# Performance work log

Hardware: AMD Instinct MI355X
Metric: run time of the kernel (lower is better)

The kernel has to match this reference:

```python
import jax, jax.numpy as jnp
import numpy as np

N_NODES = 50000
N_EDGES = 800000
HIDDEN = 128
NUM_LAYERS = 3
NEG_SLOPE = 0.2  # PyG GATConv default leaky_relu slope


def setup_inputs() -> dict:
    key = jax.random.key(0)
    ks = jax.random.split(key, 10)
    d = HIDDEN
    glorot = 1.0 / np.sqrt(d)
    inp = {
        "x": jax.random.normal(ks[0], (N_NODES, d), dtype=jnp.float32),
        "edge_index": jax.random.randint(ks[1], (2, N_EDGES), 0, N_NODES, dtype=jnp.int32),
        "edge_mask": jax.random.uniform(ks[2], (N_EDGES,), dtype=jnp.float32),
        # GATConv params (heads=1)
        "W_gat": jax.random.normal(ks[3], (d, d), dtype=jnp.float32) * glorot,
        "a_src": jax.random.normal(ks[4], (d,), dtype=jnp.float32) * glorot,
        "a_dst": jax.random.normal(ks[5], (d,), dtype=jnp.float32) * glorot,
        "b_gat": jnp.zeros((d,), dtype=jnp.float32),
        # Stacked GCNConv params
        "W_gcn": jax.random.normal(ks[6], (NUM_LAYERS, d, d), dtype=jnp.float32) * glorot,
        "b_gcn": jnp.zeros((NUM_LAYERS, d), dtype=jnp.float32),
    }
    return inp


def _seg_softmax(e, seg, n):
    m = jax.ops.segment_max(e, seg, num_segments=n)
    p = jnp.exp(e - m[seg])
    s = jax.ops.segment_sum(p, seg, num_segments=n)
    return p / s[seg]


def reference(x, edge_index, edge_mask, W_gat, a_src, a_dst, b_gat, W_gcn, b_gcn):
    N = x.shape[0]
    loops = jnp.arange(N, dtype=edge_index.dtype)
    src = jnp.concatenate([edge_index[0], loops])  # [E+N] with self loops
    dst = jnp.concatenate([edge_index[1], loops])

    # --- GATConv (heads=1, add_self_loops=True); edge_attr ignored (edge_dim=None) ---
    xp = x @ W_gat                                      # [N, d]
    e = jax.nn.leaky_relu((xp @ a_src)[src] + (xp @ a_dst)[dst], NEG_SLOPE)
    alpha = _seg_softmax(e, dst, N)                     # segment softmax over incoming edges
    h = jax.ops.segment_sum(alpha[:, None] * xp[src], dst, num_segments=N) + b_gat

    # --- GCN normalization with edge_mask as edge_weight (self-loop weight = 1) ---
    w = jnp.concatenate([edge_mask, jnp.ones((N,), dtype=edge_mask.dtype)])
    deg = jax.ops.segment_sum(w, dst, num_segments=N)
    dinv = jnp.where(deg > 0, jax.lax.rsqrt(jnp.maximum(deg, 1e-12)), 0.0)
    norm = dinv[src] * w * dinv[dst]                    # [E+N]

    outs = [h]
    for l in range(NUM_LAYERS):
        z = outs[-1] @ W_gcn[l]                         # [N, d]
        z = jax.ops.segment_sum(norm[:, None] * z[src], dst, num_segments=N) + b_gcn[l]
        outs.append(jax.nn.relu(z))

    # JumpingKnowledge 'max': elementwise max over layer outputs
    return jnp.max(jnp.stack(outs, axis=0), axis=0)
```

## Files before the change

### kernel.cpp

```cpp
#include <hip/hip_runtime.h>

#define HIDDEN 128
#define NEG_SLOPE 0.2f
#define P_SORT 256

typedef unsigned short ushort_t;
typedef __attribute__((ext_vector_type(8))) short short8;
typedef __attribute__((ext_vector_type(4))) float floatx4;

static inline size_t align_up(size_t x, size_t a){ return (x + a - 1) & ~(a - 1); }

__device__ __forceinline__ ushort_t f2b(float f){
  unsigned u = __float_as_uint(f);
  unsigned r = (u + 0x7FFFu + ((u >> 16) & 1u)) >> 16;
  return (ushort_t)r;
}

__device__ __forceinline__ void fma8(float* acc, uint4 v, float a){
  acc[0] += a * __uint_as_float(v.x << 16);
  acc[1] += a * __uint_as_float(v.x & 0xFFFF0000u);
  acc[2] += a * __uint_as_float(v.y << 16);
  acc[3] += a * __uint_as_float(v.y & 0xFFFF0000u);
  acc[4] += a * __uint_as_float(v.z << 16);
  acc[5] += a * __uint_as_float(v.z & 0xFFFF0000u);
  acc[6] += a * __uint_as_float(v.w << 16);
  acc[7] += a * __uint_as_float(v.w & 0xFFFF0000u);
}

__device__ __forceinline__ uint4 pack8(const float* f){
  uint4 u;
  u.x = (unsigned)f2b(f[0]) | ((unsigned)f2b(f[1]) << 16);
  u.y = (unsigned)f2b(f[2]) | ((unsigned)f2b(f[3]) << 16);
  u.z = (unsigned)f2b(f[4]) | ((unsigned)f2b(f[5]) << 16);
  u.w = (unsigned)f2b(f[6]) | ((unsigned)f2b(f[7]) << 16);
  return u;
}


__global__ __launch_bounds__(256) void k_b1cnt(const int* __restrict__ dst,
                                               int* __restrict__ bcnt,
                                               int E, int epb, int nbkt){
  __shared__ unsigned c[256];
  int t = threadIdx.x;
  c[t] = 0;
  __syncthreads();
  int e0 = blockIdx.x * epb;
  int e1 = min(E, e0 + epb);
  for (int e = e0 + t; e < e1; e += 256) atomicAdd(&c[dst[e] >> 8], 1u);
  __syncthreads();
  if (t < nbkt) bcnt[t * P_SORT + blockIdx.x] = (int)c[t];
}

__global__ void k_scan1(const int* __restrict__ in, int* __restrict__ incl,
                        int* __restrict__ blockSums, int M){
  __shared__ int sd[256];
  int t = threadIdx.x;
  int i = blockIdx.x*256 + t;
  int v = (i < M) ? in[i] : 0;
  sd[t] = v; __syncthreads();
  for (int off = 1; off < 256; off <<= 1){
    int add = (t >= off) ? sd[t-off] : 0;
    __syncthreads();
    sd[t] += add;
    __syncthreads();
  }
  if (i < M) incl[i] = sd[t];
  if (t == 255) blockSums[blockIdx.x] = sd[255];
}

__global__ void k_scan2(const int* __restrict__ blockSums, int* __restrict__ blockOffs, int nb){
  __shared__ int sd[256];
  __shared__ int carry;
  int t = threadIdx.x;
  if (t == 0) carry = 0;
  __syncthreads();
  for (int base = 0; base < nb; base += 256){
    int i = base + t;
    int v = (i < nb) ? blockSums[i] : 0;
    sd[t] = v; __syncthreads();
    for (int off = 1; off < 256; off <<= 1){
      int add = (t >= off) ? sd[t-off] : 0;
      __syncthreads();
      sd[t] += add;
      __syncthreads();
    }
    if (i < nb) blockOffs[i] = carry + sd[t] - v;
    __syncthreads();
    if (t == 0) carry += sd[255];
    __syncthreads();
  }
}

__global__ void k_scanex(int* __restrict__ arr, const int* __restrict__ in,
                         const int* __restrict__ blockOffs, int M){
  int i = blockIdx.x*256 + threadIdx.x;
  if (i < M) arr[i] = arr[i] - in[i] + blockOffs[blockIdx.x];
}

__global__ __launch_bounds__(256) void k_b1place(const int* __restrict__ src,
                                                 const int* __restrict__ dst,
                                                 const float* __restrict__ w,
                                                 const int* __restrict__ ebase,
                                                 unsigned* __restrict__ tpk,
                                                 float* __restrict__ tw,
                                                 int E, int epb){
  __shared__ unsigned c[256];
  int t = threadIdx.x;
  c[t] = 0;
  __syncthreads();
  int e0 = blockIdx.x * epb;
  int e1 = min(E, e0 + epb);
  for (int e = e0 + t; e < e1; e += 256){
    int d = dst[e];
    int b = d >> 8;
    unsigned r = atomicAdd(&c[b], 1u);
    int pos = ebase[b * P_SORT + blockIdx.x] + (int)r;
    tpk[pos] = (unsigned)src[e] | ((unsigned)(d & 255) << 16);
    tw[pos]  = w[e];
  }
}

__global__ __launch_bounds__(256) void k_b2(const unsigned* __restrict__ tpk,
                                            const float* __restrict__ tw,
                                            const int* __restrict__ ebase,
                                            int* __restrict__ col_src,
                                            float* __restrict__ col_w,
                                            int* __restrict__ rowp,
                                            float* __restrict__ dinv,
                                            int N, int E, int nbkt){
  __shared__ unsigned hcnt[256];
  __shared__ int sd[256];
  __shared__ int lofs[256];
  __shared__ unsigned rcnt[256];
  __shared__ float wsum[256];
  int b = blockIdx.x, t = threadIdx.x;
  int e0 = ebase[b * P_SORT];
  int e1 = (b + 1 < nbkt) ? ebase[(b + 1) * P_SORT] : E;
  hcnt[t] = 0; rcnt[t] = 0; wsum[t] = 0.f;
  __syncthreads();
  for (int e = e0 + t; e < e1; e += 256) atomicAdd(&hcnt[(tpk[e] >> 16) & 255u], 1u);
  __syncthreads();
  int v = (int)hcnt[t];
  sd[t] = v; __syncthreads();
  for (int off = 1; off < 256; off <<= 1){
    int add = (t >= off) ? sd[t-off] : 0;
    __syncthreads();
    sd[t] += add;
    __syncthreads();
  }
  lofs[t] = sd[t] - v;
  int node = b*256 + t;
  if (node < N) rowp[node] = e0 + sd[t] - v;
  if (b == 0 && t == 0) rowp[N] = E;
  __syncthreads();
  for (int e = e0 + t; e < e1; e += 256){
    unsigned pk = tpk[e];
    float wv = tw[e];
    unsigned dl = (pk >> 16) & 255u;
    unsigned r = atomicAdd(&rcnt[dl], 1u);
    int pos = e0 + lofs[dl] + (int)r;
    col_src[pos] = (int)(pk & 0xFFFFu);
    col_w[pos]   = wv;
    atomicAdd(&wsum[dl], wv);
  }
  __syncthreads();
  if (node < N) dinv[node] = rsqrtf(wsum[t] + 1.0f);
}


__global__ void k_cast_x(const float* __restrict__ x, unsigned* __restrict__ xb, long n2){
  long i = (long)blockIdx.x*256 + threadIdx.x;
  if (i >= n2) return;
  float2 v = ((const float2*)x)[i];
  xb[i] = (unsigned)f2b(v.x) | ((unsigned)f2b(v.y) << 16);
}

__global__ void k_cast_w(const float* __restrict__ Wg, const float* __restrict__ Wc,
                         ushort_t* __restrict__ Wt){
  int i = blockIdx.x*256 + threadIdx.x;
  int mat = i >> 14, idx = i & 16383;
  int k = idx >> 7, n = idx & 127;
  float v = (mat == 0) ? Wg[idx] : Wc[(mat-1)*16384 + idx];
  Wt[mat*16384 + n*128 + k] = f2b(v);
}

__global__ __launch_bounds__(256) void k_gemm(const ushort_t* __restrict__ A,
                                              const ushort_t* __restrict__ Wt,
                                              ushort_t* __restrict__ C, int M){
  int wave = threadIdx.x >> 6, l = threadIdx.x & 63;
  int q = l >> 4, lm = l & 15;
  int rowBase = blockIdx.x*128 + wave*32;
  floatx4 acc[2][8];
  #pragma unroll
  for (int mt = 0; mt < 2; mt++)
    #pragma unroll
    for (int nt = 0; nt < 8; nt++) acc[mt][nt] = (floatx4){0.f,0.f,0.f,0.f};

  #pragma unroll
  for (int kc = 0; kc < 4; kc++){
    int k0 = kc*32 + q*8;
    short8 a[2];
    #pragma unroll
    for (int mt = 0; mt < 2; mt++){
      long r = rowBase + mt*16 + lm;
      if (r < M) a[mt] = *(const short8*)(A + r*128 + k0);
      else       a[mt] = (short8){0,0,0,0,0,0,0,0};
    }
    #pragma unroll
    for (int nt = 0; nt < 8; nt++){
      short8 b = *(const short8*)(Wt + (nt*16 + lm)*128 + k0);
      acc[0][nt] = __builtin_amdgcn_mfma_f32_16x16x32_bf16(a[0], b, acc[0][nt], 0, 0, 0);
      acc[1][nt] = __builtin_amdgcn_mfma_f32_16x16x32_bf16(a[1], b, acc[1][nt], 0, 0, 0);
    }
  }
  #pragma unroll
  for (int mt = 0; mt < 2; mt++){
    #pragma unroll
    for (int r = 0; r < 4; r++){
      long row = rowBase + mt*16 + q*4 + r;
      if (row < M){
        #pragma unroll
        for (int nt = 0; nt < 8; nt++)
          C[row*128 + nt*16 + lm] = f2b(acc[mt][nt][r]);
      }
    }
  }
}

__global__ void k_sdots(const unsigned* __restrict__ xb, const float* __restrict__ a_src,
                        const float* __restrict__ a_dst, const float* __restrict__ dinv,
                        float2* __restrict__ attr, float* __restrict__ sdst, int N){
  int n = blockIdx.x*4 + (threadIdx.x >> 6);
  int lane = threadIdx.x & 63;
  if (n >= N) return;
  unsigned w = xb[(size_t)n*64 + lane];
  float v0 = __uint_as_float(w << 16);
  float v1 = __uint_as_float(w & 0xFFFF0000u);
  float2 as = ((const float2*)a_src)[lane];
  float2 ad = ((const float2*)a_dst)[lane];
  float ps = v0*as.x + v1*as.y;
  float pd = v0*ad.x + v1*ad.y;
  #pragma unroll
  for (int off = 32; off >= 1; off >>= 1){
    ps += __shfl_xor(ps, off, 64);
    pd += __shfl_xor(pd, off, 64);
  }
  if (lane == 0){
    attr[n] = make_float2(ps, dinv[n]);
    sdst[n] = pd;
  }
}

__global__ void k_post(const int* __restrict__ rowp, const int* __restrict__ col_src,
                       const float* __restrict__ col_w, const float2* __restrict__ attr,
                       const float* __restrict__ sdst, const float* __restrict__ dinv,
                       int2* __restrict__ col_en, int2* __restrict__ col_ea,
                       float* __restrict__ selfa, int N){
  int n = blockIdx.x*4 + (threadIdx.x >> 6);
  int l = threadIdx.x & 63;
  if (n >= N) return;
  int rs = rowp[n], re = rowp[n+1];
  float dn = dinv[n], sdd = sdst[n];
  float es = attr[n].x + sdd;
  es = (es >= 0.f) ? es : NEG_SLOPE*es;
  float m = es;
  float lg[3];
  int r = 0;
  for (int j = rs + l; j < re; j += 64, r++){
    int s = col_src[j];
    float w = col_w[j];
    float2 a = attr[s];
    col_en[j] = make_int2(s, __float_as_int(a.y * w * dn));
    float ee = a.x + sdd;
    ee = (ee >= 0.f) ? ee : NEG_SLOPE*ee;
    if (r < 3) lg[r] = ee;
    m = fmaxf(m, ee);
  }
  #pragma unroll
  for (int off = 32; off >= 1; off >>= 1) m = fmaxf(m, __shfl_xor(m, off, 64));
  float ps = 0.f;
  r = 0;
  for (int j = rs + l; j < re; j += 64, r++){
    float ee;
    if (r < 3) ee = lg[r];
    else {
      float2 a = attr[col_en[j].x];
      ee = a.x + sdd;
      ee = (ee >= 0.f) ? ee : NEG_SLOPE*ee;
    }
    ps += __expf(ee - m);
  }
  #pragma unroll
  for (int off = 32; off >= 1; off >>= 1) ps += __shfl_xor(ps, off, 64);
  ps += __expf(es - m);
  float inv = 1.f / ps;
  r = 0;
  for (int j = rs + l; j < re; j += 64, r++){
    float ee;
    if (r < 3) ee = lg[r];
    else {
      float2 a = attr[col_en[j].x];
      ee = a.x + sdd;
      ee = (ee >= 0.f) ? ee : NEG_SLOPE*ee;
    }
    col_ea[j] = make_int2(col_en[j].x, __float_as_int(__expf(ee - m) * inv));
  }
  if (l == 0) selfa[n] = __expf(es - m) * inv;
}

template<int MODE>
__global__ __launch_bounds__(256) void k_agg(const ushort_t* __restrict__ feat,
                                             const int* __restrict__ rowp,
                                             const int2* __restrict__ col,
                                             const float* __restrict__ selfc,
                                             const float* __restrict__ bias,
                                             ushort_t* __restrict__ out,
                                             float* __restrict__ y, int N){
  int n = blockIdx.x*4 + (threadIdx.x >> 6);
  if (n >= N) return;
  int l = threadIdx.x & 63;
  int sub = l >> 4, q = l & 15;
  int rs = rowp[n], re = rowp[n+1];
  const uint4* f16 = (const uint4*)feat;
  float acc[8] = {0.f,0.f,0.f,0.f,0.f,0.f,0.f,0.f};
  for (int base = rs; base < re; base += 8){
    int ea = base + sub;
    int eb = ea + 4;
    int ca = min(ea, re-1), cb = min(eb, re-1);
    int2 pa = col[ca];
    int2 pb = col[cb];
    float aa = (ea < re) ? __int_as_float(pa.y) : 0.f;
    float ab = (eb < re) ? __int_as_float(pb.y) : 0.f;
    uint4 va = f16[(size_t)pa.x*16 + q];
    uint4 vb = f16[(size_t)pb.x*16 + q];
    fma8(acc, va, aa);
    fma8(acc, vb, ab);
  }
  #pragma unroll
  for (int j = 0; j < 8; j++){
    acc[j] += __shfl_xor(acc[j], 16, 64);
    acc[j] += __shfl_xor(acc[j], 32, 64);
  }
  if (sub == 0){
    float sc = selfc[n];
    if (MODE == 1) sc = sc * sc;
    uint4 v = f16[(size_t)n*16 + q];
    fma8(acc, v, sc);
    float4 b0 = ((const float4*)bias)[q*2];
    float4 b1 = ((const float4*)bias)[q*2 + 1];
    acc[0]+=b0.x; acc[1]+=b0.y; acc[2]+=b0.z; acc[3]+=b0.w;
    acc[4]+=b1.x; acc[5]+=b1.y; acc[6]+=b1.z; acc[7]+=b1.w;
    if (MODE == 1){
      #pragma unroll
      for (int j = 0; j < 8; j++) acc[j] = fmaxf(acc[j], 0.f);
    }
    ((uint4*)out)[(size_t)n*16 + q] = pack8(acc);
    float4* y4 = (float4*)y;
    size_t yi = (size_t)n*32 + q*2;
    float4 n0 = make_float4(acc[0], acc[1], acc[2], acc[3]);
    float4 n1 = make_float4(acc[4], acc[5], acc[6], acc[7]);
    if (MODE == 0){
      y4[yi] = n0; y4[yi+1] = n1;
    } else {
      float4 y0 = y4[yi], y1 = y4[yi+1];
      y0.x=fmaxf(y0.x,n0.x); y0.y=fmaxf(y0.y,n0.y); y0.z=fmaxf(y0.z,n0.z); y0.w=fmaxf(y0.w,n0.w);
      y1.x=fmaxf(y1.x,n1.x); y1.y=fmaxf(y1.y,n1.y); y1.z=fmaxf(y1.z,n1.z); y1.w=fmaxf(y1.w,n1.w);
      y4[yi] = y0; y4[yi+1] = y1;
    }
  }
}

extern "C" void kernel_launch(void* const* d_in, const int* in_sizes, int n_in,
                              void* d_out, int out_size, void* d_ws, size_t ws_size,
                              hipStream_t stream){
  const float* x      = (const float*)d_in[0];
  const int*   eidx   = (const int*)d_in[1];
  const float* emask  = (const float*)d_in[2];
  const float* W_gat  = (const float*)d_in[3];
  const float* a_src  = (const float*)d_in[4];
  const float* a_dst  = (const float*)d_in[5];
  const float* b_gat  = (const float*)d_in[6];
  const float* W_gcn  = (const float*)d_in[7];
  const float* b_gcn  = (const float*)d_in[8];
  int N = in_sizes[0] / HIDDEN;
  int E = in_sizes[1] / 2;
  const int* src = eidx;
  const int* dst = eidx + E;

  char* p = (char*)d_ws;
  auto carve = [&](size_t bytes)->char*{ char* q = p; p += align_up(bytes, 512); return q; };
  ushort_t* xb   = (ushort_t*)carve((size_t)N*HIDDEN*2);
  ushort_t* zb   = (ushort_t*)carve((size_t)N*HIDDEN*2);
  ushort_t* hb   = (ushort_t*)carve((size_t)N*HIDDEN*2);
  ushort_t* Wt   = (ushort_t*)carve((size_t)4*HIDDEN*HIDDEN*2);
  float2* attr   = (float2*)carve((size_t)N*8);
  float* sdst    = (float*)carve((size_t)N*4);
  float* dinv    = (float*)carve((size_t)N*4);
  float* selfa   = (float*)carve((size_t)N*4);
  int*   rowp    = (int*)  carve((size_t)(N+1)*4);
  int*   col_src = (int*)  carve((size_t)E*4);
  float* col_w   = (float*)carve((size_t)E*4);
  int2*  col_en  = (int2*) carve((size_t)E*8);
  int2*  col_ea  = (int2*) carve((size_t)E*8);
  unsigned* tpk  = (unsigned*)carve((size_t)E*4);
  float* tw      = (float*)carve((size_t)E*4);
  int nbkt = (N + 255) >> 8;
  int M    = nbkt * P_SORT;
  int*   bcnt  = (int*)carve((size_t)M*4);
  int*   ebase = (int*)carve((size_t)M*4);
  int nbs = (M + 255) / 256;
  int*   blockSums = (int*)carve((size_t)nbs*4);
  int*   blockOffs = (int*)carve((size_t)nbs*4);
  (void)ws_size; (void)n_in; (void)out_size;

  int epb = (E + P_SORT - 1) / P_SORT;
  int gb  = (N + 127) / 128;
  int nwb = (N + 3) / 4;
  long n2 = (long)N*64;
  int cb  = (int)((n2 + 255) / 256);

  k_b1cnt  <<<P_SORT, 256, 0, stream>>>(dst, bcnt, E, epb, nbkt);
  k_scan1  <<<nbs, 256, 0, stream>>>(bcnt, ebase, blockSums, M);
  k_scan2  <<<1,   256, 0, stream>>>(blockSums, blockOffs, nbs);
  k_scanex <<<nbs, 256, 0, stream>>>(ebase, bcnt, blockOffs, M);
  k_b1place<<<P_SORT, 256, 0, stream>>>(src, dst, emask, ebase, tpk, tw, E, epb);
  k_b2     <<<nbkt, 256, 0, stream>>>(tpk, tw, ebase, col_src, col_w, rowp, dinv, N, E, nbkt);

  k_cast_x<<<cb, 256, 0, stream>>>(x, (unsigned*)xb, n2);
  k_cast_w<<<(4*HIDDEN*HIDDEN)/256, 256, 0, stream>>>(W_gat, W_gcn, Wt);

  k_gemm <<<gb, 256, 0, stream>>>(xb, Wt, zb, N);
  k_sdots<<<nwb,256, 0, stream>>>((const unsigned*)zb, a_src, a_dst, dinv, attr, sdst, N);
  k_post <<<nwb,256, 0, stream>>>(rowp, col_src, col_w, attr, sdst, dinv,
                                  col_en, col_ea, selfa, N);

  k_agg<0><<<nwb, 256, 0, stream>>>(zb, rowp, col_ea, selfa,
                                    b_gat, hb, (float*)d_out, N);
  for (int l = 0; l < 3; l++){
    k_gemm<<<gb, 256, 0, stream>>>(hb, Wt + (size_t)(l+1)*HIDDEN*HIDDEN, zb, N);
    k_agg<1><<<nwb, 256, 0, stream>>>(zb, rowp, col_en, dinv,
                                      b_gcn + (size_t)l*HIDDEN, hb, (float*)d_out, N);
  }
}
```

Baseline: 377.3 us.

## Fuse attention dots into GEMM, single-pass softmax, deeper gather unroll in aggregation

The attention source/destination dot products now run in the GEMM epilogue from the fp32 accumulators, which removes the separate k_sdots kernel and its re-read of the projected features. The edge softmax in k_post becomes a single pass that stores unnormalized exponentials without subtracting the segment max. The per-node 1/sum normalization moves into the aggregation kernel. The aggregation loop now issues four gathers per lane per iteration instead of two, for more memory-level parallelism. Dropping the max subtraction risks overflow or precision loss when logits are large, and the dots now use fp32 rather than bf16-rounded features.

Result: faster. 360.1 us (-4.6%).

```diff
diff --git a/kernel.cpp b/kernel.cpp
--- a/kernel.cpp
+++ b/kernel.cpp
@@ -184,9 +184,15 @@
   Wt[mat*16384 + n*128 + k] = f2b(v);
 }
 
+template<int DOTS>
 __global__ __launch_bounds__(256) void k_gemm(const ushort_t* __restrict__ A,
                                               const ushort_t* __restrict__ Wt,
-                                              ushort_t* __restrict__ C, int M){
+                                              ushort_t* __restrict__ C,
+                                              const float* __restrict__ a_src,
+                                              const float* __restrict__ a_dst,
+                                              const float* __restrict__ dinv,
+                                              float2* __restrict__ attr,
+                                              float* __restrict__ sdst, int M){
   int wave = threadIdx.x >> 6, l = threadIdx.x & 63;
   int q = l >> 4, lm = l & 15;
   int rowBase = blockIdx.x*128 + wave*32;
@@ -225,29 +231,32 @@
       }
     }
   }
-}
-
-__global__ void k_sdots(const unsigned* __restrict__ xb, const float* __restrict__ a_src,
-                        const float* __restrict__ a_dst, const float* __restrict__ dinv,
-                        float2* __restrict__ attr, float* __restrict__ sdst, int N){
-  int n = blockIdx.x*4 + (threadIdx.x >> 6);
-  int lane = threadIdx.x & 63;
-  if (n >= N) return;
-  unsigned w = xb[(size_t)n*64 + lane];
-  float v0 = __uint_as_float(w << 16);
-  float v1 = __uint_as_float(w & 0xFFFF0000u);
-  float2 as = ((const float2*)a_src)[lane];
-  float2 ad = ((const float2*)a_dst)[lane];
-  float ps = v0*as.x + v1*as.y;
-  float pd = v0*ad.x + v1*ad.y;
-  #pragma unroll
-  for (int off = 32; off >= 1; off >>= 1){
-    ps += __shfl_xor(ps, off, 64);
-    pd += __shfl_xor(pd, off, 64);
-  }
-  if (lane == 0){
-    attr[n] = make_float2(ps, dinv[n]);
-    sdst[n] = pd;
+  if (DOTS){
+    float as8[8], ad8[8];
+    #pragma unroll
+    for (int nt = 0; nt < 8; nt++){ as8[nt] = a_src[nt*16 + lm]; ad8[nt] = a_dst[nt*16 + lm]; }
+    #pragma unroll
+    for (int mt = 0; mt < 2; mt++){
+      #pragma unroll
+      for (int r = 0; r < 4; r++){
+        float ps = 0.f, pd = 0.f;
+        #pragma unroll
+        for (int nt = 0; nt < 8; nt++){
+          ps += acc[mt][nt][r] * as8[nt];
+          pd += acc[mt][nt][r] * ad8[nt];
+        }
+        #pragma unroll
+        for (int off = 1; off <= 8; off <<= 1){
+          ps += __shfl_xor(ps, off, 64);
+          pd += __shfl_xor(pd, off, 64);
+        }
+        long row = rowBase + mt*16 + q*4 + r;
+        if (lm == 0 && row < M){
+          attr[row] = make_float2(ps, dinv[row]);
+          sdst[row] = pd;
+        }
+      }
+    }
   }
 }
 
@@ -255,7 +264,7 @@
                        const float* __restrict__ col_w, const float2* __restrict__ attr,
                        const float* __restrict__ sdst, const float* __restrict__ dinv,
                        int2* __restrict__ col_en, int2* __restrict__ col_ea,
-                       float* __restrict__ selfa, int N){
+                       float2* __restrict__ nparm, int N){
   int n = blockIdx.x*4 + (threadIdx.x >> 6);
   int l = threadIdx.x & 63;
   if (n >= N) return;
@@ -263,56 +272,33 @@
   float dn = dinv[n], sdd = sdst[n];
   float es = attr[n].x + sdd;
   es = (es >= 0.f) ? es : NEG_SLOPE*es;
-  float m = es;
-  float lg[3];
-  int r = 0;
-  for (int j = rs + l; j < re; j += 64, r++){
+  float pself = __expf(es);
+  float ps = 0.f;
+  for (int j = rs + l; j < re; j += 64){
     int s = col_src[j];
     float w = col_w[j];
     float2 a = attr[s];
     col_en[j] = make_int2(s, __float_as_int(a.y * w * dn));
     float ee = a.x + sdd;
     ee = (ee >= 0.f) ? ee : NEG_SLOPE*ee;
-    if (r < 3) lg[r] = ee;
-    m = fmaxf(m, ee);
-  }
-  #pragma unroll
-  for (int off = 32; off >= 1; off >>= 1) m = fmaxf(m, __shfl_xor(m, off, 64));
-  float ps = 0.f;
-  r = 0;
-  for (int j = rs + l; j < re; j += 64, r++){
-    float ee;
-    if (r < 3) ee = lg[r];
-    else {
-      float2 a = attr[col_en[j].x];
-      ee = a.x + sdd;
-      ee = (ee >= 0.f) ? ee : NEG_SLOPE*ee;
-    }
-    ps += __expf(ee - m);
+    float pe = __expf(ee);
+    ps += pe;
+    col_ea[j] = make_int2(s, __float_as_int(pe));
   }
   #pragma unroll
   for (int off = 32; off >= 1; off >>= 1) ps += __shfl_xor(ps, off, 64);
-  ps += __expf(es - m);
-  float inv = 1.f / ps;
-  r = 0;
-  for (int j = rs + l; j < re; j += 64, r++){
-    float ee;
-    if (r < 3) ee = lg[r];
-    else {
-      float2 a = attr[col_en[j].x];
-      ee = a.x + sdd;
-      ee = (ee >= 0.f) ? ee : NEG_SLOPE*ee;
-    }
-    col_ea[j] = make_int2(col_en[j].x, __float_as_int(__expf(ee - m) * inv));
-  }
-  if (l == 0) selfa[n] = __expf(es - m) * inv;
+  if (l == 0){
+    float inv = 1.f / (ps + pself);
+    nparm[n] = make_float2(inv, pself * inv);
+  }
 }
 
 template<int MODE>
 __global__ __launch_bounds__(256) void k_agg(const ushort_t* __restrict__ feat,
                                              const int* __restrict__ rowp,
                                              const int2* __restrict__ col,
-                                             const float* __restrict__ selfc,
+                                             const float2* __restrict__ np,
+                                             const float* __restrict__ dinv,
                                              const float* __restrict__ bias,
                                              ushort_t* __restrict__ out,
                                              float* __restrict__ y, int N){
@@ -323,18 +309,20 @@
   int rs = rowp[n], re = rowp[n+1];
   const uint4* f16 = (const uint4*)feat;
   float acc[8] = {0.f,0.f,0.f,0.f,0.f,0.f,0.f,0.f};
-  for (int base = rs; base < re; base += 8){
-    int ea = base + sub;
-    int eb = ea + 4;
-    int ca = min(ea, re-1), cb = min(eb, re-1);
-    int2 pa = col[ca];
-    int2 pb = col[cb];
-    float aa = (ea < re) ? __int_as_float(pa.y) : 0.f;
-    float ab = (eb < re) ? __int_as_float(pb.y) : 0.f;
-    uint4 va = f16[(size_t)pa.x*16 + q];
-    uint4 vb = f16[(size_t)pb.x*16 + q];
-    fma8(acc, va, aa);
-    fma8(acc, vb, ab);
+  for (int base = rs; base < re; base += 16){
+    int2 p[4]; float a[4];
+    #pragma unroll
+    for (int j = 0; j < 4; j++){
+      int e = base + sub + 4*j;
+      int cc = min(e, re-1);
+      p[j] = col[cc];
+      a[j] = (e < re) ? __int_as_float(p[j].y) : 0.f;
+    }
+    uint4 v[4];
+    #pragma unroll
+    for (int j = 0; j < 4; j++) v[j] = f16[(size_t)p[j].x*16 + q];
+    #pragma unroll
+    for (int j = 0; j < 4; j++) fma8(acc, v[j], a[j]);
   }
   #pragma unroll
   for (int j = 0; j < 8; j++){
@@ -342,8 +330,16 @@
     acc[j] += __shfl_xor(acc[j], 32, 64);
   }
   if (sub == 0){
-    float sc = selfc[n];
-    if (MODE == 1) sc = sc * sc;
+    float sc;
+    if (MODE == 0){
+      float2 pp = np[n];
+      #pragma unroll
+      for (int j = 0; j < 8; j++) acc[j] *= pp.x;
+      sc = pp.y;
+    } else {
+      float di = dinv[n];
+      sc = di * di;
+    }
     uint4 v = f16[(size_t)n*16 + q];
     fma8(acc, v, sc);
     float4 b0 = ((const float4*)bias)[q*2];
@@ -394,9 +390,9 @@
   ushort_t* hb   = (ushort_t*)carve((size_t)N*HIDDEN*2);
   ushort_t* Wt   = (ushort_t*)carve((size_t)4*HIDDEN*HIDDEN*2);
   float2* attr   = (float2*)carve((size_t)N*8);
+  float2* nparm  = (float2*)carve((size_t)N*8);
   float* sdst    = (float*)carve((size_t)N*4);
   float* dinv    = (float*)carve((size_t)N*4);
-  float* selfa   = (float*)carve((size_t)N*4);
   int*   rowp    = (int*)  carve((size_t)(N+1)*4);
   int*   col_src = (int*)  carve((size_t)E*4);
   float* col_w   = (float*)carve((size_t)E*4);
@@ -429,16 +425,16 @@
   k_cast_x<<<cb, 256, 0, stream>>>(x, (unsigned*)xb, n2);
   k_cast_w<<<(4*HIDDEN*HIDDEN)/256, 256, 0, stream>>>(W_gat, W_gcn, Wt);
 
-  k_gemm <<<gb, 256, 0, stream>>>(xb, Wt, zb, N);
-  k_sdots<<<nwb,256, 0, stream>>>((const unsigned*)zb, a_src, a_dst, dinv, attr, sdst, N);
-  k_post <<<nwb,256, 0, stream>>>(rowp, col_src, col_w, attr, sdst, dinv,
-                                  col_en, col_ea, selfa, N);
-
-  k_agg<0><<<nwb, 256, 0, stream>>>(zb, rowp, col_ea, selfa,
+  k_gemm<1><<<gb, 256, 0, stream>>>(xb, Wt, zb, a_src, a_dst, dinv, attr, sdst, N);
+  k_post<<<nwb, 256, 0, stream>>>(rowp, col_src, col_w, attr, sdst, dinv,
+                                  col_en, col_ea, nparm, N);
+
+  k_agg<0><<<nwb, 256, 0, stream>>>(zb, rowp, col_ea, nparm, dinv,
                                     b_gat, hb, (float*)d_out, N);
   for (int l = 0; l < 3; l++){
-    k_gemm<<<gb, 256, 0, stream>>>(hb, Wt + (size_t)(l+1)*HIDDEN*HIDDEN, zb, N);
-    k_agg<1><<<nwb, 256, 0, stream>>>(zb, rowp, col_en, dinv,
+    k_gemm<0><<<gb, 256, 0, stream>>>(hb, Wt + (size_t)(l+1)*HIDDEN*HIDDEN, zb,
+                                      a_src, a_dst, dinv, attr, sdst, N);
+    k_agg<1><<<nwb, 256, 0, stream>>>(zb, rowp, col_en, nparm, dinv,
                                       b_gcn + (size_t)l*HIDDEN, hb, (float*)d_out, N);
   }
 }
```
